# Kernel tuning notes

Hardware: AMD Instinct MI355X
Metric: run time of the kernel (lower is better)

Reference implementation:

```python
import jax, jax.numpy as jnp
import numpy as np

N, E, F_IN, HID, HEADS, G = 50000, 800000, 128, 32, 8, 64
NEG_SLOPE = 0.2  # PyG GATConv default leaky_relu slope


def gat_conv(x, src, dst, W, att_src, att_dst, bias, heads, out_ch):
    """PyG-style GATConv (concat=True, self-loops already included in src/dst)."""
    n = x.shape[0]
    h = (x @ W).reshape(n, heads, out_ch)            # [N,H,C]
    a_src = jnp.sum(h * att_src, axis=-1)            # [N,H]
    a_dst = jnp.sum(h * att_dst, axis=-1)            # [N,H]
    e = jax.nn.leaky_relu(a_src[src] + a_dst[dst], NEG_SLOPE)  # [Et,H]
    # segment softmax over incoming edges of each destination node
    m = jax.ops.segment_max(e, dst, num_segments=n)
    e = jnp.exp(e - m[dst])
    denom = jax.ops.segment_sum(e, dst, num_segments=n)
    alpha = e / (denom[dst] + 1e-16)                 # [Et,H]
    msg = h[src] * alpha[:, :, None]                 # [Et,H,C]
    out = jax.ops.segment_sum(msg, dst, num_segments=n)
    return out.reshape(n, heads * out_ch) + bias


def setup_inputs() -> dict:
    key = jax.random.key(0)
    ks = jax.random.split(key, 16)
    x = jax.random.normal(ks[0], (N, F_IN), dtype=jnp.float32)
    edge_index = jax.random.randint(ks[1], (2, E), 0, N, dtype=jnp.int64)
    batch = jnp.sort(jax.random.randint(ks[2], (N,), 0, G, dtype=jnp.int64))
    s = 0.05
    params = dict(
        W1=jax.random.normal(ks[3], (F_IN, HEADS * HID), jnp.float32) * s,
        att_src1=jax.random.normal(ks[4], (1, HEADS, HID), jnp.float32) * s,
        att_dst1=jax.random.normal(ks[5], (1, HEADS, HID), jnp.float32) * s,
        b1=jnp.zeros((HEADS * HID,), jnp.float32),
        W2=jax.random.normal(ks[6], (HEADS * HID, HID), jnp.float32) * s,
        att_src2=jax.random.normal(ks[7], (1, 1, HID), jnp.float32) * s,
        att_dst2=jax.random.normal(ks[8], (1, 1, HID), jnp.float32) * s,
        b2=jnp.zeros((HID,), jnp.float32),
        Wo=jax.random.normal(ks[9], (HID, 1), jnp.float32) * s,
        bo=jnp.zeros((1,), jnp.float32),
    )
    return dict(x=x, edge_index=edge_index, batch=batch, **params)


def reference(x, edge_index, batch, W1, att_src1, att_dst1, b1,
              W2, att_src2, att_dst2, b2, Wo, bo):
    # add self loops (PyG GATConv default add_self_loops=True)
    loop = jnp.arange(N, dtype=edge_index.dtype)
    src = jnp.concatenate([edge_index[0], loop])
    dst = jnp.concatenate([edge_index[1], loop])

    h = jax.nn.elu(gat_conv(x, src, dst, W1, att_src1, att_dst1, b1, HEADS, HID))
    # dropout p=0.2 is identity in eval mode
    h = jax.nn.elu(gat_conv(h, src, dst, W2, att_src2, att_dst2, b2, 1, HID))

    # global mean pool over graphs
    sums = jax.ops.segment_sum(h, batch, num_segments=G)          # [G,HID]
    cnts = jax.ops.segment_sum(jnp.ones((N,), h.dtype), batch, num_segments=G)
    pooled = sums / jnp.maximum(cnts, 1.0)[:, None]

    return jax.nn.sigmoid(pooled @ Wo + bo)                        # [G,1]
```

## Files before the change

### kernel.cpp

```cpp
#include <hip/hip_runtime.h>
#include <hip/hip_bf16.h>
#include <math.h>

#define NN 50000
#define NE 800000
#define ET (NE + NN)
#define FIN 128
#define HEADS 8
#define HID 32
#define C1 (HEADS * HID)
#define NG 64
#define NEG 0.2f

#define EPB 2048
#define NBKT 782
#define CAP 2048

typedef __attribute__((ext_vector_type(8))) unsigned short ushort8_t;
typedef __attribute__((ext_vector_type(4))) unsigned short ushort4_t;
typedef __attribute__((ext_vector_type(2))) float float2_t;
typedef __attribute__((ext_vector_type(8))) short bf16x8;
typedef __attribute__((ext_vector_type(4))) float f32x4;

__device__ __forceinline__ float lrelu(float v) { return v > 0.f ? v : NEG * v; }
__device__ __forceinline__ float elu1(float v)  { return v > 0.f ? v : expm1f(v); }
__device__ __forceinline__ unsigned short f2bf(float f) {
    __hip_bfloat16 b = __float2bfloat16(f);
    return *reinterpret_cast<unsigned short*>(&b);
}
__device__ __forceinline__ float bf2f(unsigned short u) {
    return __uint_as_float(((unsigned)u) << 16);
}
__device__ __forceinline__ void dec_fma16(uint4 r, float e, float* acc) {
    float2_t f;
    f = __builtin_amdgcn_cvt_pk_f32_fp8((int)r.x, false); acc[0] += e * f.x; acc[1] += e * f.y;
    f = __builtin_amdgcn_cvt_pk_f32_fp8((int)r.x, true);  acc[2] += e * f.x; acc[3] += e * f.y;
    f = __builtin_amdgcn_cvt_pk_f32_fp8((int)r.y, false); acc[4] += e * f.x; acc[5] += e * f.y;
    f = __builtin_amdgcn_cvt_pk_f32_fp8((int)r.y, true);  acc[6] += e * f.x; acc[7] += e * f.y;
    f = __builtin_amdgcn_cvt_pk_f32_fp8((int)r.z, false); acc[8] += e * f.x; acc[9] += e * f.y;
    f = __builtin_amdgcn_cvt_pk_f32_fp8((int)r.z, true);  acc[10] += e * f.x; acc[11] += e * f.y;
    f = __builtin_amdgcn_cvt_pk_f32_fp8((int)r.w, false); acc[12] += e * f.x; acc[13] += e * f.y;
    f = __builtin_amdgcn_cvt_pk_f32_fp8((int)r.w, true);  acc[14] += e * f.x; acc[15] += e * f.y;
}

__global__ __launch_bounds__(256) void bkt_scatter_kernel(const int* __restrict__ ei,
                                                          int* __restrict__ bcur,
                                                          uint2* __restrict__ bkt) {
    __shared__ int es[EPB];
    __shared__ int ed[EPB];
    __shared__ int lh[NBKT];
    int t = threadIdx.x;
    int base = blockIdx.x * EPB;
    int nloc = ET - base; if (nloc > EPB) nloc = EPB;
    for (int i = t; i < NBKT; i += 256) lh[i] = 0;
    __syncthreads();
    for (int k = t; k < nloc; k += 256) {
        int i = base + k;
        int s, d;
        if (i < NE) { s = ei[i]; d = ei[NE + i]; }
        else        { s = i - NE; d = s; }
        es[k] = s; ed[k] = d;
        atomicAdd(&lh[d >> 6], 1);
    }
    __syncthreads();
    for (int i = t; i < NBKT; i += 256) {
        int c = lh[i];
        lh[i] = c ? atomicAdd(&bcur[i], c) : 0;
    }
    __syncthreads();
    for (int k = t; k < nloc; k += 256) {
        int d = ed[k];
        int b = d >> 6;
        int pos = atomicAdd(&lh[b], 1);
        if (pos < CAP) bkt[(size_t)b * CAP + pos] = make_uint2((unsigned)es[k], (unsigned)d);
    }
}

__global__ __launch_bounds__(256) void bkt_scan_kernel(const int* __restrict__ bcur,
                                                       int* __restrict__ bbase,
                                                       int* __restrict__ rowptr) {
    __shared__ int wsum[4];
    int t = threadIdx.x, lane = t & 63, w = t >> 6;
    int idx = t * 4;
    int a0 = (idx + 0 < NBKT) ? bcur[idx + 0] : 0;
    int a1 = (idx + 1 < NBKT) ? bcur[idx + 1] : 0;
    int a2 = (idx + 2 < NBKT) ? bcur[idx + 2] : 0;
    int a3 = (idx + 3 < NBKT) ? bcur[idx + 3] : 0;
    int v = a0 + a1 + a2 + a3;
    int inc = v;
    #pragma unroll
    for (int off = 1; off < 64; off <<= 1) {
        int u = __shfl_up(inc, off, 64);
        if (lane >= off) inc += u;
    }
    if (lane == 63) wsum[w] = inc;
    __syncthreads();
    int woff = 0;
    #pragma unroll
    for (int i = 0; i < 4; ++i) if (i < w) woff += wsum[i];
    int excl = woff + inc - v;
    if (idx + 0 < NBKT) bbase[idx + 0] = excl;
    if (idx + 1 < NBKT) bbase[idx + 1] = excl + a0;
    if (idx + 2 < NBKT) bbase[idx + 2] = excl + a0 + a1;
    if (idx + 3 < NBKT) bbase[idx + 3] = excl + a0 + a1 + a2;
    if (t == 255) rowptr[NN] = woff + inc;
}

__global__ __launch_bounds__(256) void csr_kernel(const uint2* __restrict__ bkt,
                                                  const int* __restrict__ bcur,
                                                  const int* __restrict__ bbase,
                                                  int* __restrict__ rowptr,
                                                  int* __restrict__ ssrc) {
    __shared__ int nb[64];
    __shared__ int nc[64];
    int b = blockIdx.x, t = threadIdx.x;
    int cnt = bcur[b]; if (cnt > CAP) cnt = CAP;
    int gbase = bbase[b];
    if (t < 64) nc[t] = 0;
    __syncthreads();
    const uint2* e = bkt + (size_t)b * CAP;
    for (int k = t; k < cnt; k += 256)
        atomicAdd(&nc[e[k].y & 63], 1);
    __syncthreads();
    if (t < 64) {
        int v = nc[t];
        int inc = v;
        #pragma unroll
        for (int off = 1; off < 64; off <<= 1) {
            int u = __shfl_up(inc, off, 64);
            if (t >= off) inc += u;
        }
        int start = gbase + inc - v;
        nb[t] = start;
        int node = b * 64 + t;
        if (node < NN) rowptr[node] = start;
    }
    __syncthreads();
    for (int k = t; k < cnt; k += 256) {
        uint2 ed = e[k];
        int pos = atomicAdd(&nb[ed.y & 63], 1);
        ssrc[pos] = (int)ed.x;
    }
}

__global__ __launch_bounds__(256) void cvt_x_kernel(const float* __restrict__ x,
                                                    unsigned short* __restrict__ xb) {
    int i = (blockIdx.x * 256 + threadIdx.x) * 8;
    if (i >= NN * FIN) return;
    float4 f0 = *(const float4*)&x[i];
    float4 f1 = *(const float4*)&x[i + 4];
    ushort8_t o;
    o[0] = f2bf(f0.x); o[1] = f2bf(f0.y); o[2] = f2bf(f0.z); o[3] = f2bf(f0.w);
    o[4] = f2bf(f1.x); o[5] = f2bf(f1.y); o[6] = f2bf(f1.z); o[7] = f2bf(f1.w);
    *(ushort8_t*)&xb[i] = o;
}

__global__ __launch_bounds__(256) void cvt_w1_kernel(const float* __restrict__ W1,
                                                     unsigned short* __restrict__ w1swz) {
    int t = blockIdx.x * 256 + threadIdx.x;
    int fid = t >> 6, lane = t & 63;
    int tnt = fid >> 2, ks = fid & 3;
    int n = tnt * 16 + (lane & 15);
    int k0 = ks * 32 + (lane >> 4) * 8;
    ushort8_t o;
    #pragma unroll
    for (int j = 0; j < 8; ++j) o[j] = f2bf(W1[(k0 + j) * C1 + n]);
    *(ushort8_t*)&w1swz[(size_t)(fid * 64 + lane) * 8] = o;
}

__global__ __launch_bounds__(256) void gemm1_kernel(
        const unsigned short* __restrict__ xb, const unsigned short* __restrict__ w1swz,
        const float* __restrict__ attS, const float* __restrict__ attD,
        unsigned char* __restrict__ h1f8, float* __restrict__ aS, float* __restrict__ aD) {
    __shared__ float lds[4 * 16 * 132];
    int t = threadIdx.x, w = t >> 6, lane = t & 63;
    int mh = w & 1, nh = w >> 1;
    int m0 = blockIdx.x * 64 + mh * 32;
    int l15 = lane & 15, l4 = lane >> 4;

    f32x4 acc[2][8];
    #pragma unroll
    for (int mt = 0; mt < 2; ++mt)
        #pragma unroll
        for (int nt = 0; nt < 8; ++nt)
            acc[mt][nt] = (f32x4){0.f, 0.f, 0.f, 0.f};

    int ra = m0 + l15;       if (ra >= NN) ra = NN - 1;
    int rb = m0 + 16 + l15;  if (rb >= NN) rb = NN - 1;
    const unsigned short* a0p = xb + (size_t)ra * FIN + l4 * 8;
    const unsigned short* a1p = xb + (size_t)rb * FIN + l4 * 8;

    #pragma unroll
    for (int ks = 0; ks < 4; ++ks) {
        bf16x8 af0 = *(const bf16x8*)(a0p + ks * 32);
        bf16x8 af1 = *(const bf16x8*)(a1p + ks * 32);
        #pragma unroll
        for (int nt = 0; nt < 8; ++nt) {
            bf16x8 bf = *(const bf16x8*)&w1swz[(size_t)(((nh * 8 + nt) * 4 + ks) * 64 + lane) * 8];
            acc[0][nt] = __builtin_amdgcn_mfma_f32_16x16x32_bf16(af0, bf, acc[0][nt], 0, 0, 0);
            acc[1][nt] = __builtin_amdgcn_mfma_f32_16x16x32_bf16(af1, bf, acc[1][nt], 0, 0, 0);
        }
    }

    float* wl = lds + w * 16 * 132;
    #pragma unroll
    for (int mt = 0; mt < 2; ++mt) {
        __syncthreads();
        #pragma unroll
        for (int nt = 0; nt < 8; ++nt)
            #pragma unroll
            for (int r = 0; r < 4; ++r)
                wl[(l4 * 4 + r) * 132 + nt * 16 + l15] = acc[mt][nt][r];
        __syncthreads();
        int row_g = m0 + mt * 16 + l15;
        int cch = l4;
        float v[32];
        #pragma unroll
        for (int i = 0; i < 8; ++i) {
            float4 f = *(const float4*)&wl[l15 * 132 + cch * 32 + i * 4];
            v[i * 4 + 0] = f.x; v[i * 4 + 1] = f.y; v[i * 4 + 2] = f.z; v[i * 4 + 3] = f.w;
        }
        if (row_g < NN) {
            unsigned pk[8];
            #pragma unroll
            for (int i = 0; i < 8; ++i) {
                int p = __builtin_amdgcn_cvt_pk_fp8_f32(v[i * 4 + 0], v[i * 4 + 1], 0, false);
                p = __builtin_amdgcn_cvt_pk_fp8_f32(v[i * 4 + 2], v[i * 4 + 3], p, true);
                pk[i] = (unsigned)p;
            }
            size_t base = (size_t)row_g * C1 + nh * 128 + cch * 32;
            *(uint4*)&h1f8[base]      = make_uint4(pk[0], pk[1], pk[2], pk[3]);
            *(uint4*)&h1f8[base + 16] = make_uint4(pk[4], pk[5], pk[6], pk[7]);
            int h = nh * 4 + cch;
            float ps = 0.f, pd = 0.f;
            #pragma unroll
            for (int i = 0; i < 32; ++i) {
                ps += v[i] * attS[h * 32 + i];
                pd += v[i] * attD[h * 32 + i];
            }
            aS[row_g * HEADS + h] = ps;
            aD[row_g * HEADS + h] = pd;
        }
    }
}

__global__ __launch_bounds__(256) void agg1_kernel(
        const int* __restrict__ rowptr, const int* __restrict__ ssrc,
        const float* __restrict__ aS, const float* __restrict__ aD,
        const unsigned char* __restrict__ h1f8, const float* __restrict__ b1,
        unsigned short* __restrict__ z1b) {
    int d = (blockIdx.x * 256 + threadIdx.x) >> 6;
    int lane = threadIdx.x & 63;
    if (d >= NN) return;
    int start = rowptr[d], end = rowptr[d + 1];
    int q = lane >> 4, sl = lane & 15;
    int h = sl >> 1;
    float adh = aD[d * HEADS + h];
    float acc[16];
    #pragma unroll
    for (int i = 0; i < 16; ++i) acc[i] = 0.f;
    float den = 0.f;
    int j = start + q;
    for (; j + 4 < end; j += 8) {
        int s0 = ssrc[j], s1 = ssrc[j + 4];
        uint4 r0 = *(const uint4*)&h1f8[(size_t)s0 * C1 + sl * 16];
        uint4 r1 = *(const uint4*)&h1f8[(size_t)s1 * C1 + sl * 16];
        float e0 = __expf(lrelu(aS[s0 * HEADS + h] + adh));
        float e1 = __expf(lrelu(aS[s1 * HEADS + h] + adh));
        den += e0 + e1;
        dec_fma16(r0, e0, acc);
        dec_fma16(r1, e1, acc);
    }
    for (; j < end; j += 4) {
        int s = ssrc[j];
        uint4 r = *(const uint4*)&h1f8[(size_t)s * C1 + sl * 16];
        float e = __expf(lrelu(aS[s * HEADS + h] + adh));
        den += e;
        dec_fma16(r, e, acc);
    }
    den += __shfl_xor(den, 16, 64);
    den += __shfl_xor(den, 32, 64);
    #pragma unroll
    for (int i = 0; i < 16; ++i) {
        acc[i] += __shfl_xor(acc[i], 16, 64);
        acc[i] += __shfl_xor(acc[i], 32, 64);
    }
    float invd = 1.f / (den + 1e-16f);
    int cb = sl * 16 + q * 4;
    float4 bb = *(const float4*)&b1[cb];
    ushort4_t o;
    o[0] = f2bf(elu1(acc[q * 4 + 0] * invd + bb.x));
    o[1] = f2bf(elu1(acc[q * 4 + 1] * invd + bb.y));
    o[2] = f2bf(elu1(acc[q * 4 + 2] * invd + bb.z));
    o[3] = f2bf(elu1(acc[q * 4 + 3] * invd + bb.w));
    *(ushort4_t*)&z1b[(size_t)d * C1 + cb] = o;
}

__global__ __launch_bounds__(256) void gemm2_kernel(
        const unsigned short* __restrict__ z1b, const float* __restrict__ W2,
        const float* __restrict__ attS, const float* __restrict__ attD,
        unsigned short* __restrict__ h2b, float* __restrict__ aS2, float* __restrict__ aD2) {
    __shared__ float zs[32 * 260];
    __shared__ float wc[64 * HID];
    int t = threadIdx.x;
    int n0 = blockIdx.x * 32;
    {
        int f = t * 32, r = f >> 8, c = f & 255;
        if (n0 + r < NN) {
            const ushort8_t* zr = (const ushort8_t*)&z1b[(size_t)(n0 + r) * C1 + c];
            #pragma unroll
            for (int i = 0; i < 4; ++i) {
                ushort8_t u = zr[i];
                *(float4*)&zs[r * 260 + c + i * 8] =
                    make_float4(bf2f(u[0]), bf2f(u[1]), bf2f(u[2]), bf2f(u[3]));
                *(float4*)&zs[r * 260 + c + i * 8 + 4] =
                    make_float4(bf2f(u[4]), bf2f(u[5]), bf2f(u[6]), bf2f(u[7]));
            }
        } else {
            float4 z = make_float4(0.f, 0.f, 0.f, 0.f);
            #pragma unroll
            for (int i = 0; i < 8; ++i) *(float4*)&zs[r * 260 + c + i * 4] = z;
        }
    }
    int tn = t >> 3, tc = t & 7;
    float acc[4] = {0.f, 0.f, 0.f, 0.f};
    for (int kb = 0; kb < 4; ++kb) {
        __syncthreads();
        {
            const float4* w4 = (const float4*)(W2 + kb * 64 * HID);
            float4* s4 = (float4*)wc;
            s4[t] = w4[t]; s4[t + 256] = w4[t + 256];
        }
        __syncthreads();
        for (int k = 0; k < 64; ++k) {
            float zv = zs[tn * 260 + kb * 64 + k];
            float4 w = *(const float4*)&wc[k * HID + tc * 4];
            acc[0] += zv * w.x; acc[1] += zv * w.y;
            acc[2] += zv * w.z; acc[3] += zv * w.w;
        }
    }
    int n = n0 + tn;
    float ps = 0.f, pd = 0.f;
    #pragma unroll
    for (int j = 0; j < 4; ++j) { ps += acc[j] * attS[tc * 4 + j]; pd += acc[j] * attD[tc * 4 + j]; }
    ps += __shfl_xor(ps, 1, 64); ps += __shfl_xor(ps, 2, 64); ps += __shfl_xor(ps, 4, 64);
    pd += __shfl_xor(pd, 1, 64); pd += __shfl_xor(pd, 2, 64); pd += __shfl_xor(pd, 4, 64);
    if (n < NN) {
        ushort4_t o;
        o[0] = f2bf(acc[0]); o[1] = f2bf(acc[1]); o[2] = f2bf(acc[2]); o[3] = f2bf(acc[3]);
        *(ushort4_t*)&h2b[(size_t)n * HID + tc * 4] = o;
        if (tc == 0) { aS2[n] = ps; aD2[n] = pd; }
    }
}

__global__ __launch_bounds__(256) void agg2_kernel(
        const int* __restrict__ rowptr, const int* __restrict__ ssrc,
        const float* __restrict__ aS, const float* __restrict__ aD,
        const unsigned short* __restrict__ h2b, const float* __restrict__ b2,
        float* __restrict__ z2) {
    int d = (blockIdx.x * 256 + threadIdx.x) >> 6;
    int lane = threadIdx.x & 63;
    if (d >= NN) return;
    int start = rowptr[d], end = rowptr[d + 1];
    int q = lane >> 4, sl = lane & 15;
    float adv = aD[d];
    float a0 = 0.f, a1 = 0.f, den = 0.f;
    int j = start + q;
    for (; j + 4 < end; j += 8) {
        int s0 = ssrc[j], s1 = ssrc[j + 4];
        unsigned r0 = *(const unsigned*)&h2b[(size_t)s0 * HID + sl * 2];
        unsigned r1 = *(const unsigned*)&h2b[(size_t)s1 * HID + sl * 2];
        float e0 = __expf(lrelu(aS[s0] + adv));
        float e1 = __expf(lrelu(aS[s1] + adv));
        den += e0 + e1;
        a0 += e0 * bf2f((unsigned short)(r0 & 0xffff));
        a1 += e0 * bf2f((unsigned short)(r0 >> 16));
        a0 += e1 * bf2f((unsigned short)(r1 & 0xffff));
        a1 += e1 * bf2f((unsigned short)(r1 >> 16));
    }
    for (; j < end; j += 4) {
        int s = ssrc[j];
        unsigned r = *(const unsigned*)&h2b[(size_t)s * HID + sl * 2];
        float e = __expf(lrelu(aS[s] + adv));
        den += e;
        a0 += e * bf2f((unsigned short)(r & 0xffff));
        a1 += e * bf2f((unsigned short)(r >> 16));
    }
    den += __shfl_xor(den, 16, 64);
    den += __shfl_xor(den, 32, 64);
    a0 += __shfl_xor(a0, 16, 64); a0 += __shfl_xor(a0, 32, 64);
    a1 += __shfl_xor(a1, 16, 64); a1 += __shfl_xor(a1, 32, 64);
    if (q == 0) {
        float invd = 1.f / (den + 1e-16f);
        float2 o;
        o.x = elu1(a0 * invd + b2[sl * 2]);
        o.y = elu1(a1 * invd + b2[sl * 2 + 1]);
        *(float2*)&z2[(size_t)d * HID + sl * 2] = o;
    }
}

__global__ __launch_bounds__(256) void pool_partial_kernel(
        const float* __restrict__ z2, const int* __restrict__ batch,
        float* __restrict__ pooled) {
    __shared__ float sm[256];
    int g = blockIdx.x >> 4, slice = blockIdx.x & 15;
    int t = threadIdx.x;
    int lo = 0, hi = NN;
    while (lo < hi) { int m = (lo + hi) >> 1; if (batch[m] < g) lo = m + 1; else hi = m; }
    int start = lo;
    hi = NN;
    while (lo < hi) { int m = (lo + hi) >> 1; if (batch[m] < g + 1) lo = m + 1; else hi = m; }
    int end = lo;
    int len = end - start;
    int s0 = start + (int)(((long long)len * slice) >> 4);
    int s1 = start + (int)(((long long)len * (slice + 1)) >> 4);
    int c = t & 31, r = t >> 5;
    float acc = 0.f;
    for (int n = s0 + r; n < s1; n += 8)
        acc += z2[(size_t)n * HID + c];
    sm[t] = acc;
    __syncthreads();
    if (t < 32) {
        float s = 0.f;
        #pragma unroll
        for (int i = 0; i < 8; ++i) s += sm[t + 32 * i];
        atomicAdd(&pooled[g * HID + t], s);
    }
}

__global__ void pool_finish_kernel(const float* __restrict__ pooled,
                                   const int* __restrict__ batch,
                                   const float* __restrict__ Wo, const float* __restrict__ bo,
                                   float* __restrict__ out) {
    int g = threadIdx.x;
    if (g >= NG) return;
    int lo = 0, hi = NN;
    while (lo < hi) { int m = (lo + hi) >> 1; if (batch[m] < g) lo = m + 1; else hi = m; }
    int start = lo;
    hi = NN;
    while (lo < hi) { int m = (lo + hi) >> 1; if (batch[m] < g + 1) lo = m + 1; else hi = m; }
    int end = lo;
    float c = fmaxf((float)(end - start), 1.f);
    float acc = 0.f;
    for (int i = 0; i < HID; ++i) acc += (pooled[g * HID + i] / c) * Wo[i];
    acc += bo[0];
    out[g] = 1.f / (1.f + __expf(-acc));
}

extern "C" void kernel_launch(void* const* d_in, const int* in_sizes, int n_in,
                              void* d_out, int out_size, void* d_ws, size_t ws_size,
                              hipStream_t stream) {
    const float* x     = (const float*)d_in[0];
    const int*   ei    = (const int*)d_in[1];
    const int*   batch = (const int*)d_in[2];
    const float* W1    = (const float*)d_in[3];
    const float* attS1 = (const float*)d_in[4];
    const float* attD1 = (const float*)d_in[5];
    const float* b1    = (const float*)d_in[6];
    const float* W2    = (const float*)d_in[7];
    const float* attS2 = (const float*)d_in[8];
    const float* attD2 = (const float*)d_in[9];
    const float* b2    = (const float*)d_in[10];
    const float* Wo    = (const float*)d_in[11];
    const float* bo    = (const float*)d_in[12];
    float* out = (float*)d_out;

    char* p = (char*)d_ws;
    auto alloc = [&](size_t bytes) {
        char* r = p;
        p += (bytes + 255) & ~(size_t)255;
        return (void*)r;
    };
    unsigned char*  h1f8  = (unsigned char*)alloc((size_t)NN * C1);
    unsigned short* xb    = (unsigned short*)alloc((size_t)NN * FIN * 2);
    unsigned short* w1swz = (unsigned short*)alloc((size_t)FIN * C1 * 2);
    unsigned short* z1b   = (unsigned short*)alloc((size_t)NN * C1 * 2);
    unsigned short* h2b   = (unsigned short*)alloc((size_t)NN * HID * 2);
    float* aS1    = (float*)alloc((size_t)NN * HEADS * 4);
    float* aD1    = (float*)alloc((size_t)NN * HEADS * 4);
    float* z2     = (float*)alloc((size_t)NN * HID * 4);
    float* aS2    = (float*)alloc((size_t)NN * 4);
    float* aD2    = (float*)alloc((size_t)NN * 4);
    int*   rowptr = (int*)alloc((size_t)(NN + 1) * 4);
    int*   ssrc   = (int*)alloc((size_t)ET * 4);
    uint2* bkt    = (uint2*)alloc((size_t)NBKT * CAP * 8);
    int*   bbase  = (int*)alloc((size_t)NBKT * 4);
    int*   bcur   = (int*)alloc((size_t)NBKT * 4);
    float* pooled = (float*)alloc((size_t)NG * HID * 4);
    size_t zero_bytes = (size_t)(p - (char*)bcur);

    hipMemsetAsync(bcur, 0, zero_bytes, stream);
    bkt_scatter_kernel<<<(ET + EPB - 1) / EPB, 256, 0, stream>>>(ei, bcur, bkt);
    bkt_scan_kernel<<<1, 256, 0, stream>>>(bcur, bbase, rowptr);
    csr_kernel<<<NBKT, 256, 0, stream>>>(bkt, bcur, bbase, rowptr, ssrc);
    cvt_x_kernel<<<(NN * FIN / 8 + 255) / 256, 256, 0, stream>>>(x, xb);
    cvt_w1_kernel<<<16, 256, 0, stream>>>(W1, w1swz);
    gemm1_kernel<<<(NN + 63) / 64, 256, 0, stream>>>(xb, w1swz, attS1, attD1, h1f8, aS1, aD1);
    agg1_kernel<<<(NN * 64) / 256, 256, 0, stream>>>(rowptr, ssrc, aS1, aD1, h1f8, b1, z1b);
    gemm2_kernel<<<(NN + 31) / 32, 256, 0, stream>>>(z1b, W2, attS2, attD2, h2b, aS2, aD2);
    agg2_kernel<<<(NN * 64 + 255) / 256, 256, 0, stream>>>(rowptr, ssrc, aS2, aD2, h2b, b2, z2);
    pool_partial_kernel<<<NG * 16, 256, 0, stream>>>(z2, batch, pooled);
    pool_finish_kernel<<<1, 64, 0, stream>>>(pooled, batch, Wo, bo, out);
}
```

Baseline: 266.9 us.

## Fuse x conversion into GEMM1, MFMA GEMM2, pack bucket entries, vectorize aggregation

```diff
diff --git a/kernel.cpp b/kernel.cpp
--- a/kernel.cpp
+++ b/kernel.cpp
@@ -12,7 +12,7 @@
 #define NG 64
 #define NEG 0.2f
 
-#define EPB 2048
+#define EPB 4096
 #define NBKT 782
 #define CAP 2048
 
@@ -31,23 +31,22 @@
 __device__ __forceinline__ float bf2f(unsigned short u) {
     return __uint_as_float(((unsigned)u) << 16);
 }
-__device__ __forceinline__ void dec_fma16(uint4 r, float e, float* acc) {
-    float2_t f;
-    f = __builtin_amdgcn_cvt_pk_f32_fp8((int)r.x, false); acc[0] += e * f.x; acc[1] += e * f.y;
-    f = __builtin_amdgcn_cvt_pk_f32_fp8((int)r.x, true);  acc[2] += e * f.x; acc[3] += e * f.y;
-    f = __builtin_amdgcn_cvt_pk_f32_fp8((int)r.y, false); acc[4] += e * f.x; acc[5] += e * f.y;
-    f = __builtin_amdgcn_cvt_pk_f32_fp8((int)r.y, true);  acc[6] += e * f.x; acc[7] += e * f.y;
-    f = __builtin_amdgcn_cvt_pk_f32_fp8((int)r.z, false); acc[8] += e * f.x; acc[9] += e * f.y;
-    f = __builtin_amdgcn_cvt_pk_f32_fp8((int)r.z, true);  acc[10] += e * f.x; acc[11] += e * f.y;
-    f = __builtin_amdgcn_cvt_pk_f32_fp8((int)r.w, false); acc[12] += e * f.x; acc[13] += e * f.y;
-    f = __builtin_amdgcn_cvt_pk_f32_fp8((int)r.w, true);  acc[14] += e * f.x; acc[15] += e * f.y;
+__device__ __forceinline__ void dec_fma16(uint4 r, float e, float2_t* acc) {
+    float2_t ev = {e, e};
+    acc[0] += ev * __builtin_amdgcn_cvt_pk_f32_fp8((int)r.x, false);
+    acc[1] += ev * __builtin_amdgcn_cvt_pk_f32_fp8((int)r.x, true);
+    acc[2] += ev * __builtin_amdgcn_cvt_pk_f32_fp8((int)r.y, false);
+    acc[3] += ev * __builtin_amdgcn_cvt_pk_f32_fp8((int)r.y, true);
+    acc[4] += ev * __builtin_amdgcn_cvt_pk_f32_fp8((int)r.z, false);
+    acc[5] += ev * __builtin_amdgcn_cvt_pk_f32_fp8((int)r.z, true);
+    acc[6] += ev * __builtin_amdgcn_cvt_pk_f32_fp8((int)r.w, false);
+    acc[7] += ev * __builtin_amdgcn_cvt_pk_f32_fp8((int)r.w, true);
 }
 
 __global__ __launch_bounds__(256) void bkt_scatter_kernel(const int* __restrict__ ei,
                                                           int* __restrict__ bcur,
-                                                          uint2* __restrict__ bkt) {
-    __shared__ int es[EPB];
-    __shared__ int ed[EPB];
+                                                          unsigned* __restrict__ bkt) {
+    __shared__ unsigned ep[EPB];
     __shared__ int lh[NBKT];
     int t = threadIdx.x;
     int base = blockIdx.x * EPB;
@@ -59,7 +58,7 @@
         int s, d;
         if (i < NE) { s = ei[i]; d = ei[NE + i]; }
         else        { s = i - NE; d = s; }
-        es[k] = s; ed[k] = d;
+        ep[k] = (unsigned)s | ((unsigned)(d & 63) << 16) | ((unsigned)(d >> 6) << 22);
         atomicAdd(&lh[d >> 6], 1);
     }
     __syncthreads();
@@ -69,10 +68,10 @@
     }
     __syncthreads();
     for (int k = t; k < nloc; k += 256) {
-        int d = ed[k];
-        int b = d >> 6;
+        unsigned v = ep[k];
+        int b = (int)(v >> 22);
         int pos = atomicAdd(&lh[b], 1);
-        if (pos < CAP) bkt[(size_t)b * CAP + pos] = make_uint2((unsigned)es[k], (unsigned)d);
+        if (pos < CAP) bkt[(size_t)b * CAP + pos] = v & 0x3FFFFFu;
     }
 }
 
@@ -106,7 +105,7 @@
     if (t == 255) rowptr[NN] = woff + inc;
 }
 
-__global__ __launch_bounds__(256) void csr_kernel(const uint2* __restrict__ bkt,
+__global__ __launch_bounds__(256) void csr_kernel(const unsigned* __restrict__ bkt,
                                                   const int* __restrict__ bcur,
                                                   const int* __restrict__ bbase,
                                                   int* __restrict__ rowptr,
@@ -118,9 +117,9 @@
     int gbase = bbase[b];
     if (t < 64) nc[t] = 0;
     __syncthreads();
-    const uint2* e = bkt + (size_t)b * CAP;
+    const unsigned* e = bkt + (size_t)b * CAP;
     for (int k = t; k < cnt; k += 256)
-        atomicAdd(&nc[e[k].y & 63], 1);
+        atomicAdd(&nc[e[k] >> 16], 1);
     __syncthreads();
     if (t < 64) {
         int v = nc[t];
@@ -137,22 +136,10 @@
     }
     __syncthreads();
     for (int k = t; k < cnt; k += 256) {
-        uint2 ed = e[k];
-        int pos = atomicAdd(&nb[ed.y & 63], 1);
-        ssrc[pos] = (int)ed.x;
-    }
-}
-
-__global__ __launch_bounds__(256) void cvt_x_kernel(const float* __restrict__ x,
-                                                    unsigned short* __restrict__ xb) {
-    int i = (blockIdx.x * 256 + threadIdx.x) * 8;
-    if (i >= NN * FIN) return;
-    float4 f0 = *(const float4*)&x[i];
-    float4 f1 = *(const float4*)&x[i + 4];
-    ushort8_t o;
-    o[0] = f2bf(f0.x); o[1] = f2bf(f0.y); o[2] = f2bf(f0.z); o[3] = f2bf(f0.w);
-    o[4] = f2bf(f1.x); o[5] = f2bf(f1.y); o[6] = f2bf(f1.z); o[7] = f2bf(f1.w);
-    *(ushort8_t*)&xb[i] = o;
+        unsigned v = e[k];
+        int pos = atomicAdd(&nb[v >> 16], 1);
+        ssrc[pos] = (int)(v & 0xFFFFu);
+    }
 }
 
 __global__ __launch_bounds__(256) void cvt_w1_kernel(const float* __restrict__ W1,
@@ -168,8 +155,21 @@
     *(ushort8_t*)&w1swz[(size_t)(fid * 64 + lane) * 8] = o;
 }
 
+__global__ __launch_bounds__(256) void cvt_w2_kernel(const float* __restrict__ W2,
+                                                     unsigned short* __restrict__ w2swz) {
+    int t = blockIdx.x * 256 + threadIdx.x;
+    int fid = t >> 6, lane = t & 63;
+    int nt = fid >> 3, ks = fid & 7;
+    int n = nt * 16 + (lane & 15);
+    int k0 = ks * 32 + (lane >> 4) * 8;
+    ushort8_t o;
+    #pragma unroll
+    for (int j = 0; j < 8; ++j) o[j] = f2bf(W2[(k0 + j) * HID + n]);
+    *(ushort8_t*)&w2swz[(size_t)(fid * 64 + lane) * 8] = o;
+}
+
 __global__ __launch_bounds__(256) void gemm1_kernel(
-        const unsigned short* __restrict__ xb, const unsigned short* __restrict__ w1swz,
+        const float* __restrict__ x, const unsigned short* __restrict__ w1swz,
         const float* __restrict__ attS, const float* __restrict__ attD,
         unsigned char* __restrict__ h1f8, float* __restrict__ aS, float* __restrict__ aD) {
     __shared__ float lds[4 * 16 * 132];
@@ -187,13 +187,24 @@
 
     int ra = m0 + l15;       if (ra >= NN) ra = NN - 1;
     int rb = m0 + 16 + l15;  if (rb >= NN) rb = NN - 1;
-    const unsigned short* a0p = xb + (size_t)ra * FIN + l4 * 8;
-    const unsigned short* a1p = xb + (size_t)rb * FIN + l4 * 8;
+    const float* a0p = x + (size_t)ra * FIN + l4 * 8;
+    const float* a1p = x + (size_t)rb * FIN + l4 * 8;
 
     #pragma unroll
     for (int ks = 0; ks < 4; ++ks) {
-        bf16x8 af0 = *(const bf16x8*)(a0p + ks * 32);
-        bf16x8 af1 = *(const bf16x8*)(a1p + ks * 32);
+        float4 f00 = *(const float4*)(a0p + ks * 32);
+        float4 f01 = *(const float4*)(a0p + ks * 32 + 4);
+        float4 f10 = *(const float4*)(a1p + ks * 32);
+        float4 f11 = *(const float4*)(a1p + ks * 32 + 4);
+        bf16x8 af0, af1;
+        af0[0] = (short)f2bf(f00.x); af0[1] = (short)f2bf(f00.y);
+        af0[2] = (short)f2bf(f00.z); af0[3] = (short)f2bf(f00.w);
+        af0[4] = (short)f2bf(f01.x); af0[5] = (short)f2bf(f01.y);
+        af0[6] = (short)f2bf(f01.z); af0[7] = (short)f2bf(f01.w);
+        af1[0] = (short)f2bf(f10.x); af1[1] = (short)f2bf(f10.y);
+        af1[2] = (short)f2bf(f10.z); af1[3] = (short)f2bf(f10.w);
+        af1[4] = (short)f2bf(f11.x); af1[5] = (short)f2bf(f11.y);
+        af1[6] = (short)f2bf(f11.z); af1[7] = (short)f2bf(f11.w);
         #pragma unroll
         for (int nt = 0; nt < 8; ++nt) {
             bf16x8 bf = *(const bf16x8*)&w1swz[(size_t)(((nh * 8 + nt) * 4 + ks) * 64 + lane) * 8];
@@ -256,9 +267,9 @@
     int q = lane >> 4, sl = lane & 15;
     int h = sl >> 1;
     float adh = aD[d * HEADS + h];
-    float acc[16];
-    #pragma unroll
-    for (int i = 0; i < 16; ++i) acc[i] = 0.f;
+    float2_t acc[8];
+    #pragma unroll
+    for (int i = 0; i < 8; ++i) acc[i] = (float2_t){0.f, 0.f};
     float den = 0.f;
     int j = start + q;
     for (; j + 4 < end; j += 8) {
@@ -281,75 +292,77 @@
     den += __shfl_xor(den, 16, 64);
     den += __shfl_xor(den, 32, 64);
     #pragma unroll
-    for (int i = 0; i < 16; ++i) {
-        acc[i] += __shfl_xor(acc[i], 16, 64);
-        acc[i] += __shfl_xor(acc[i], 32, 64);
+    for (int i = 0; i < 8; ++i) {
+        acc[i].x += __shfl_xor(acc[i].x, 16, 64);
+        acc[i].y += __shfl_xor(acc[i].y, 16, 64);
+        acc[i].x += __shfl_xor(acc[i].x, 32, 64);
+        acc[i].y += __shfl_xor(acc[i].y, 32, 64);
     }
     float invd = 1.f / (den + 1e-16f);
     int cb = sl * 16 + q * 4;
     float4 bb = *(const float4*)&b1[cb];
     ushort4_t o;
-    o[0] = f2bf(elu1(acc[q * 4 + 0] * invd + bb.x));
-    o[1] = f2bf(elu1(acc[q * 4 + 1] * invd + bb.y));
-    o[2] = f2bf(elu1(acc[q * 4 + 2] * invd + bb.z));
-    o[3] = f2bf(elu1(acc[q * 4 + 3] * invd + bb.w));
+    o[0] = f2bf(elu1(acc[q * 2 + 0].x * invd + bb.x));
+    o[1] = f2bf(elu1(acc[q * 2 + 0].y * invd + bb.y));
+    o[2] = f2bf(elu1(acc[q * 2 + 1].x * invd + bb.z));
+    o[3] = f2bf(elu1(acc[q * 2 + 1].y * invd + bb.w));
     *(ushort4_t*)&z1b[(size_t)d * C1 + cb] = o;
 }
 
 __global__ __launch_bounds__(256) void gemm2_kernel(
-        const unsigned short* __restrict__ z1b, const float* __restrict__ W2,
+        const unsigned short* __restrict__ z1b, const unsigned short* __restrict__ w2swz,
         const float* __restrict__ attS, const float* __restrict__ attD,
         unsigned short* __restrict__ h2b, float* __restrict__ aS2, float* __restrict__ aD2) {
-    __shared__ float zs[32 * 260];
-    __shared__ float wc[64 * HID];
-    int t = threadIdx.x;
-    int n0 = blockIdx.x * 32;
+    __shared__ float lds[4 * 16 * 36];
+    int t = threadIdx.x, w = t >> 6, lane = t & 63;
+    int m0 = blockIdx.x * 64 + w * 16;
+    int l15 = lane & 15, l4 = lane >> 4;
+
+    f32x4 acc[2];
+    acc[0] = (f32x4){0.f, 0.f, 0.f, 0.f};
+    acc[1] = (f32x4){0.f, 0.f, 0.f, 0.f};
+
+    int ra = m0 + l15; if (ra >= NN) ra = NN - 1;
+    const unsigned short* ap = z1b + (size_t)ra * C1 + l4 * 8;
+
+    #pragma unroll
+    for (int ks = 0; ks < 8; ++ks) {
+        bf16x8 af = *(const bf16x8*)(ap + ks * 32);
+        #pragma unroll
+        for (int nt = 0; nt < 2; ++nt) {
+            bf16x8 bf = *(const bf16x8*)&w2swz[(size_t)((nt * 8 + ks) * 64 + lane) * 8];
+            acc[nt] = __builtin_amdgcn_mfma_f32_16x16x32_bf16(af, bf, acc[nt], 0, 0, 0);
+        }
+    }
+    float* wl = lds + w * 16 * 36;
+    #pragma unroll
+    for (int nt = 0; nt < 2; ++nt)
+        #pragma unroll
+        for (int r = 0; r < 4; ++r)
+            wl[(l4 * 4 + r) * 36 + nt * 16 + l15] = acc[nt][r];
+    __syncthreads();
+    int row_g = m0 + l15;
+    float v[8];
     {
-        int f = t * 32, r = f >> 8, c = f & 255;
-        if (n0 + r < NN) {
-            const ushort8_t* zr = (const ushort8_t*)&z1b[(size_t)(n0 + r) * C1 + c];
-            #pragma unroll
-            for (int i = 0; i < 4; ++i) {
-                ushort8_t u = zr[i];
-                *(float4*)&zs[r * 260 + c + i * 8] =
-                    make_float4(bf2f(u[0]), bf2f(u[1]), bf2f(u[2]), bf2f(u[3]));
-                *(float4*)&zs[r * 260 + c + i * 8 + 4] =
-                    make_float4(bf2f(u[4]), bf2f(u[5]), bf2f(u[6]), bf2f(u[7]));
-            }
-        } else {
-            float4 z = make_float4(0.f, 0.f, 0.f, 0.f);
-            #pragma unroll
-            for (int i = 0; i < 8; ++i) *(float4*)&zs[r * 260 + c + i * 4] = z;
-        }
-    }
-    int tn = t >> 3, tc = t & 7;
-    float acc[4] = {0.f, 0.f, 0.f, 0.f};
-    for (int kb = 0; kb < 4; ++kb) {
-        __syncthreads();
-        {
-            const float4* w4 = (const float4*)(W2 + kb * 64 * HID);
-            float4* s4 = (float4*)wc;
-            s4[t] = w4[t]; s4[t + 256] = w4[t + 256];
-        }
-        __syncthreads();
-        for (int k = 0; k < 64; ++k) {
-            float zv = zs[tn * 260 + kb * 64 + k];
-            float4 w = *(const float4*)&wc[k * HID + tc * 4];
-            acc[0] += zv * w.x; acc[1] += zv * w.y;
-            acc[2] += zv * w.z; acc[3] += zv * w.w;
-        }
-    }
-    int n = n0 + tn;
+        float4 f0 = *(const float4*)&wl[l15 * 36 + l4 * 8];
+        float4 f1 = *(const float4*)&wl[l15 * 36 + l4 * 8 + 4];
+        v[0] = f0.x; v[1] = f0.y; v[2] = f0.z; v[3] = f0.w;
+        v[4] = f1.x; v[5] = f1.y; v[6] = f1.z; v[7] = f1.w;
+    }
     float ps = 0.f, pd = 0.f;
     #pragma unroll
-    for (int j = 0; j < 4; ++j) { ps += acc[j] * attS[tc * 4 + j]; pd += acc[j] * attD[tc * 4 + j]; }
-    ps += __shfl_xor(ps, 1, 64); ps += __shfl_xor(ps, 2, 64); ps += __shfl_xor(ps, 4, 64);
-    pd += __shfl_xor(pd, 1, 64); pd += __shfl_xor(pd, 2, 64); pd += __shfl_xor(pd, 4, 64);
-    if (n < NN) {
-        ushort4_t o;
-        o[0] = f2bf(acc[0]); o[1] = f2bf(acc[1]); o[2] = f2bf(acc[2]); o[3] = f2bf(acc[3]);
-        *(ushort4_t*)&h2b[(size_t)n * HID + tc * 4] = o;
-        if (tc == 0) { aS2[n] = ps; aD2[n] = pd; }
+    for (int i = 0; i < 8; ++i) {
+        ps += v[i] * attS[l4 * 8 + i];
+        pd += v[i] * attD[l4 * 8 + i];
+    }
+    ps += __shfl_xor(ps, 16, 64); ps += __shfl_xor(ps, 32, 64);
+    pd += __shfl_xor(pd, 16, 64); pd += __shfl_xor(pd, 32, 64);
+    if (row_g < NN) {
+        ushort8_t o;
+        #pragma unroll
+        for (int i = 0; i < 8; ++i) o[i] = f2bf(v[i]);
+        *(ushort8_t*)&h2b[(size_t)row_g * HID + l4 * 8] = o;
+        if (l4 == 0) { aS2[row_g] = ps; aD2[row_g] = pd; }
     }
 }
 
@@ -364,7 +377,8 @@
     int start = rowptr[d], end = rowptr[d + 1];
     int q = lane >> 4, sl = lane & 15;
     float adv = aD[d];
-    float a0 = 0.f, a1 = 0.f, den = 0.f;
+    float2_t a = {0.f, 0.f};
+    float den = 0.f;
     int j = start + q;
     for (; j + 4 < end; j += 8) {
         int s0 = ssrc[j], s1 = ssrc[j + 4];
@@ -373,28 +387,28 @@
         float e0 = __expf(lrelu(aS[s0] + adv));
         float e1 = __expf(lrelu(aS[s1] + adv));
         den += e0 + e1;
-        a0 += e0 * bf2f((unsigned short)(r0 & 0xffff));
-        a1 += e0 * bf2f((unsigned short)(r0 >> 16));
-        a0 += e1 * bf2f((unsigned short)(r1 & 0xffff));
-        a1 += e1 * bf2f((unsigned short)(r1 >> 16));
+        float2_t v0 = {bf2f((unsigned short)(r0 & 0xffff)), bf2f((unsigned short)(r0 >> 16))};
+        float2_t v1 = {bf2f((unsigned short)(r1 & 0xffff)), bf2f((unsigned short)(r1 >> 16))};
+        a += (float2_t){e0, e0} * v0;
+        a += (float2_t){e1, e1} * v1;
     }
     for (; j < end; j += 4) {
         int s = ssrc[j];
         unsigned r = *(const unsigned*)&h2b[(size_t)s * HID + sl * 2];
         float e = __expf(lrelu(aS[s] + adv));
         den += e;
-        a0 += e * bf2f((unsigned short)(r & 0xffff));
-        a1 += e * bf2f((unsigned short)(r >> 16));
+        float2_t v = {bf2f((unsigned short)(r & 0xffff)), bf2f((unsigned short)(r >> 16))};
+        a += (float2_t){e, e} * v;
     }
     den += __shfl_xor(den, 16, 64);
     den += __shfl_xor(den, 32, 64);
-    a0 += __shfl_xor(a0, 16, 64); a0 += __shfl_xor(a0, 32, 64);
-    a1 += __shfl_xor(a1, 16, 64); a1 += __shfl_xor(a1, 32, 64);
+    a.x += __shfl_xor(a.x, 16, 64); a.x += __shfl_xor(a.x, 32, 64);
+    a.y += __shfl_xor(a.y, 16, 64); a.y += __shfl_xor(a.y, 32, 64);
     if (q == 0) {
         float invd = 1.f / (den + 1e-16f);
         float2 o;
-        o.x = elu1(a0 * invd + b2[sl * 2]);
-        o.y = elu1(a1 * invd + b2[sl * 2 + 1]);
+        o.x = elu1(a.x * invd + b2[sl * 2]);
+        o.y = elu1(a.y * invd + b2[sl * 2 + 1]);
         *(float2*)&z2[(size_t)d * HID + sl * 2] = o;
     }
 }
@@ -472,8 +486,8 @@
         return (void*)r;
     };
     unsigned char*  h1f8  = (unsigned char*)alloc((size_t)NN * C1);
-    unsigned short* xb    = (unsigned short*)alloc((size_t)NN * FIN * 2);
     unsigned short* w1swz = (unsigned short*)alloc((size_t)FIN * C1 * 2);
+    unsigned short* w2swz = (unsigned short*)alloc((size_t)C1 * HID * 2);
     unsigned short* z1b   = (unsigned short*)alloc((size_t)NN * C1 * 2);
     unsigned short* h2b   = (unsigned short*)alloc((size_t)NN * HID * 2);
     float* aS1    = (float*)alloc((size_t)NN * HEADS * 4);
@@ -483,7 +497,7 @@
     float* aD2    = (float*)alloc((size_t)NN * 4);
     int*   rowptr = (int*)alloc((size_t)(NN + 1) * 4);
     int*   ssrc   = (int*)alloc((size_t)ET * 4);
-    uint2* bkt    = (uint2*)alloc((size_t)NBKT * CAP * 8);
+    unsigned* bkt = (unsigned*)alloc((size_t)NBKT * CAP * 4);
     int*   bbase  = (int*)alloc((size_t)NBKT * 4);
     int*   bcur   = (int*)alloc((size_t)NBKT * 4);
     float* pooled = (float*)alloc((size_t)NG * HID * 4);
@@ -493,11 +507,11 @@
     bkt_scatter_kernel<<<(ET + EPB - 1) / EPB, 256, 0, stream>>>(ei, bcur, bkt);
     bkt_scan_kernel<<<1, 256, 0, stream>>>(bcur, bbase, rowptr);
     csr_kernel<<<NBKT, 256, 0, stream>>>(bkt, bcur, bbase, rowptr, ssrc);
-    cvt_x_kernel<<<(NN * FIN / 8 + 255) / 256, 256, 0, stream>>>(x, xb);
     cvt_w1_kernel<<<16, 256, 0, stream>>>(W1, w1swz);
-    gemm1_kernel<<<(NN + 63) / 64, 256, 0, stream>>>(xb, w1swz, attS1, attD1, h1f8, aS1, aD1);
+    cvt_w2_kernel<<<4, 256, 0, stream>>>(W2, w2swz);
+    gemm1_kernel<<<(NN + 63) / 64, 256, 0, stream>>>(x, w1swz, attS1, attD1, h1f8, aS1, aD1);
     agg1_kernel<<<(NN * 64) / 256, 256, 0, stream>>>(rowptr, ssrc, aS1, aD1, h1f8, b1, z1b);
-    gemm2_kernel<<<(NN + 31) / 32, 256, 0, stream>>>(z1b, W2, attS2, attD2, h2b, aS2, aD2);
+    gemm2_kernel<<<(NN + 63) / 64, 256, 0, stream>>>(z1b, w2swz, attS2, attD2, h2b, aS2, aD2);
     agg2_kernel<<<(NN * 64 + 255) / 256, 256, 0, stream>>>(rowptr, ssrc, aS2, aD2, h2b, b2, z2);
     pool_partial_kernel<<<NG * 16, 256, 0, stream>>>(z2, batch, pooled);
     pool_finish_kernel<<<1, 64, 0, stream>>>(pooled, batch, Wo, bo, out);
```

Result: faster. 244.0 us, median of 2 (-8.6%).
